# Optimization experiments

Measured on AMD Instinct MI355X. Metric: run time of the kernel, lower is better.

The kernel has to match this reference:

```python
import jax, jax.numpy as jnp
import numpy as np

N, E, F, H, C = 50000, 800000, 128, 4, 32
SLOPE_ATT = 0.2   # PyG GATConv default negative_slope for attention logits
SLOPE_ACT = 0.01  # torch leaky_relu default between layers


def setup_inputs() -> dict:
    key = jax.random.key(0)
    ks = jax.random.split(key, 12)
    sc = 0.1
    return {
        "x": jax.random.normal(ks[0], (N, F), jnp.float32),
        "edge_index": jax.random.randint(ks[1], (2, E), 0, N, dtype=jnp.int32),
        "W1": jax.random.normal(ks[2], (F, H * C), jnp.float32) * sc,
        "a_src1": jax.random.normal(ks[3], (H, C), jnp.float32) * sc,
        "a_dst1": jax.random.normal(ks[4], (H, C), jnp.float32) * sc,
        "b1": jnp.zeros((H * C,), jnp.float32),
        "W2": jax.random.normal(ks[5], (H * C, H * C), jnp.float32) * sc,
        "a_src2": jax.random.normal(ks[6], (H, C), jnp.float32) * sc,
        "a_dst2": jax.random.normal(ks[7], (H, C), jnp.float32) * sc,
        "b2": jnp.zeros((H * C,), jnp.float32),
        "Wfc": jax.random.normal(ks[8], (H * C, 1), jnp.float32) * sc,
        "bfc": jnp.zeros((1,), jnp.float32),
    }


def gat_layer(x, src, dst, W, a_src, a_dst, bias):
    """PyG-style GATConv: per-head linear, edge attention with leaky_relu,
    segment-softmax over incoming edges of each dst node, scatter-add aggregate."""
    n = x.shape[0]
    h = (x @ W).reshape(n, H, C)                       # [N,H,C]
    att_s = jnp.einsum('nhc,hc->nh', h, a_src)         # per-node src logits
    att_d = jnp.einsum('nhc,hc->nh', h, a_dst)         # per-node dst logits
    e = jax.nn.leaky_relu(att_s[src] + att_d[dst], SLOPE_ATT)   # [Etot,H]
    m = jax.ops.segment_max(e, dst, num_segments=n)    # stable softmax per dst
    e = jnp.exp(e - m[dst])
    z = jax.ops.segment_sum(e, dst, num_segments=n)
    alpha = e / (z[dst] + 1e-16)                       # [Etot,H]
    out = jax.ops.segment_sum(alpha[:, :, None] * h[src], dst, num_segments=n)
    return out.reshape(n, H * C) + bias                # concat heads + bias


def reference(x, edge_index, W1, a_src1, a_dst1, b1, W2, a_src2, a_dst2, b2, Wfc, bfc):
    loops = jnp.arange(N, dtype=edge_index.dtype)      # PyG adds self-loops
    src = jnp.concatenate([edge_index[0], loops])
    dst = jnp.concatenate([edge_index[1], loops])
    h = jax.nn.leaky_relu(gat_layer(x, src, dst, W1, a_src1, a_dst1, b1), SLOPE_ACT)
    h = jax.nn.leaky_relu(gat_layer(h, src, dst, W2, a_src2, a_dst2, b2), SLOPE_ACT)
    return (h @ Wfc + bfc).squeeze(-1)                 # [N]
```

## Files before the change

kernel.cpp:

```cpp
#include <hip/hip_runtime.h>
#include <hip/hip_fp16.h>

#define FD 128

typedef __attribute__((ext_vector_type(8))) short bf16x8;
typedef __attribute__((ext_vector_type(4))) float f32x4;

__device__ __forceinline__ float lrelu(float x, float s){ return x > 0.f ? x : s*x; }

__device__ __forceinline__ unsigned short f2bf(float f){
  unsigned u = __builtin_bit_cast(unsigned, f);
  return (unsigned short)((u + 0x7FFFu + ((u >> 16) & 1u)) >> 16);
}
__device__ __forceinline__ float bf2f(unsigned short h){
  unsigned u = ((unsigned)h) << 16;
  return __builtin_bit_cast(float, u);
}


__global__ __launch_bounds__(256) void count_wprep_kernel(const int* __restrict__ dst,
    int* __restrict__ counts, int E, unsigned rscale, int nchunk, int nbc,
    const float* __restrict__ W1, const float* __restrict__ W2,
    const float* __restrict__ aS1, const float* __restrict__ aD1,
    const float* __restrict__ aS2, const float* __restrict__ aD2,
    unsigned short* __restrict__ WT1, unsigned short* __restrict__ WT2)
{
  int b = blockIdx.x;
  if (b < nbc){
    int xcd = b & 7, chunk = b >> 3;
    int nv = E >> 2;
    for (int v = chunk*256 + threadIdx.x; v < nv; v += nchunk*256){
      int4 d4 = ((const int4*)dst)[v];
      #pragma unroll
      for (int t = 0; t < 4; ++t){
        int d = (&d4.x)[t];
        unsigned r = (unsigned)(((unsigned long long)(unsigned)d * rscale) >> 32);
        if ((int)r == xcd) atomicAdd(&counts[d], 1);
      }
    }
    if (chunk == 0 && threadIdx.x < (E & 3)){
      int i = (E & ~3) + threadIdx.x;
      int d = dst[i];
      unsigned r = (unsigned)(((unsigned long long)(unsigned)d * rscale) >> 32);
      if ((int)r == xcd) atomicAdd(&counts[d], 1);
    }
    return;
  }
  int id = (b - nbc)*256 + threadIdx.x;
  if (id < 32768){
    const float* W = (id < 16384) ? W1 : W2;
    unsigned short* T = (id < 16384) ? WT1 : WT2;
    int idx = id & 16383;
    int k = idx >> 7, c = idx & 127;
    int w = ((c & 7) << 4) | (c >> 3);
    int si = w*128 + (k ^ ((w & 7) << 3));
    float v = W[idx];
    unsigned short h = f2bf(v);
    T[si] = h;
    T[18432 + si] = f2bf(v - bf2f(h));
  } else if (id < 34816){
    int id2 = id - 32768;
    int layer = id2 >> 10;
    int id3 = id2 & 1023;
    int k = id3 >> 3, cc = id3 & 7;
    const float* W  = layer ? W2 : W1;
    const float* av = (cc < 4) ? (layer ? aS2 : aS1) : (layer ? aD2 : aD1);
    unsigned short* T = layer ? WT2 : WT1;
    int h = cc & 3, base = h*32;
    float acc = 0.f;
    #pragma unroll 8
    for (int c = 0; c < 32; ++c) acc += W[k*FD + base + c] * av[base + c];
    int w = 128 + cc;
    int si = w*128 + (k ^ ((w & 7) << 3));
    unsigned short hh = f2bf(acc);
    T[si] = hh;
    T[18432 + si] = f2bf(acc - bf2f(hh));
  } else if (id < 36864){
    int id2 = id - 34816;
    int layer = id2 >> 10;
    int id3 = id2 & 1023;
    int w = 136 + (id3 >> 7), k = id3 & 127;
    unsigned short* T = layer ? WT2 : WT1;
    int si = w*128 + (k ^ ((w & 7) << 3));
    T[si] = 0;
    T[18432 + si] = 0;
  }
}

__global__ __launch_bounds__(512) void scan1_kernel(const int* __restrict__ counts,
    int* __restrict__ offsets, int* __restrict__ blocksum, int n){
  __shared__ int wsum[8];
  int tid = threadIdx.x, lane = tid & 63, wv = tid >> 6;
  int i = blockIdx.x*512 + tid;
  int v = (i < n) ? counts[i] + 1 : 0;
  int incl = v;
  #pragma unroll
  for (int off = 1; off < 64; off <<= 1){
    int t = __shfl_up(incl, off);
    if (lane >= off) incl += t;
  }
  if (lane == 63) wsum[wv] = incl;
  __syncthreads();
  if (wv == 0 && lane < 8){
    int s = wsum[lane];
    #pragma unroll
    for (int off = 1; off < 8; off <<= 1){
      int t = __shfl_up(s, off);
      if (lane >= off) s += t;
    }
    wsum[lane] = s;
  }
  __syncthreads();
  int woff = (wv > 0) ? wsum[wv-1] : 0;
  incl += woff;
  if (i < n) offsets[i] = incl;
  if (tid == 511) blocksum[blockIdx.x] = incl;
}

__global__ __launch_bounds__(64) void scan2_kernel(int* __restrict__ blocksum,
    int* __restrict__ offsets, int nb, int n){
  int lane = threadIdx.x;
  int i0 = 2*lane, i1 = 2*lane + 1;
  int v0 = (i0 < nb) ? blocksum[i0] : 0;
  int v1 = (i1 < nb) ? blocksum[i1] : 0;
  int pair = v0 + v1;
  int incl = pair;
  #pragma unroll
  for (int off = 1; off < 64; off <<= 1){
    int t = __shfl_up(incl, off);
    if (lane >= off) incl += t;
  }
  int excl = incl - pair;
  if (i0 < nb) blocksum[i0] = excl;
  if (i1 < nb) blocksum[i1] = excl + v0;
  if (lane == 63) offsets[n] = incl;
}

__global__ __launch_bounds__(512) void scan3_kernel(const int* __restrict__ counts,
    int* __restrict__ offsets, const int* __restrict__ blocksum,
    int* __restrict__ csr, int n){
  int i = blockIdx.x*512 + threadIdx.x;
  if (i >= n) return;
  int v = counts[i] + 1;
  int gl = offsets[i] + blocksum[blockIdx.x];
  offsets[i] = gl - v;
  csr[gl - 1] = i;
}

__global__ __launch_bounds__(256) void fill_part_kernel(const int* __restrict__ ei,
    const int* __restrict__ offsets, int* __restrict__ counts, int* __restrict__ csr,
    int E, unsigned rscale, int nchunk){
  int b = blockIdx.x;
  int xcd = b & 7, chunk = b >> 3;
  int nv = E >> 2;
  for (int v = chunk*256 + threadIdx.x; v < nv; v += nchunk*256){
    int4 s4 = ((const int4*)ei)[v];
    int4 d4 = ((const int4*)(ei + E))[v];
    #pragma unroll
    for (int t = 0; t < 4; ++t){
      int d = (&d4.x)[t];
      unsigned r = (unsigned)(((unsigned long long)(unsigned)d * rscale) >> 32);
      if ((int)r == xcd){
        int c = atomicSub(&counts[d], 1) - 1;
        csr[offsets[d] + c] = (&s4.x)[t];
      }
    }
  }
  if (chunk == 0 && threadIdx.x < (E & 3)){
    int i = (E & ~3) + threadIdx.x;
    int d = ei[E + i];
    unsigned r = (unsigned)(((unsigned long long)(unsigned)d * rscale) >> 32);
    if ((int)r == xcd){
      int c = atomicSub(&counts[d], 1) - 1;
      csr[offsets[d] + c] = ei[i];
    }
  }
}

template<int SPLITIN>
__global__ __launch_bounds__(256) void gemm_mfma_kernel(
    const float* __restrict__ Xf,
    const unsigned short* __restrict__ Xh, const unsigned short* __restrict__ Xl,
    const unsigned short* __restrict__ WT,
    uint4* __restrict__ H16, float* __restrict__ attS, float* __restrict__ attD, int n)
{
  __shared__ unsigned short smem[36864];
  int tid = threadIdx.x;
  int wv = tid >> 6, lane = tid & 63;
  int g = lane >> 4, r = lane & 15;
  int rbase = blockIdx.x*64 + wv*16;
  int arow = rbase + r; if (arow >= n) arow = n - 1;

  {
    const uint4* src = (const uint4*)WT;
    uint4* dst = (uint4*)smem;
    #pragma unroll
    for (int i = 0; i < 18; ++i) dst[tid + i*256] = src[tid + i*256];
  }

  bf16x8 Ah[4], Al[4];
  if (SPLITIN){
    const bf16x8* ph = (const bf16x8*)(Xh + (size_t)arow*FD);
    const bf16x8* pl = (const bf16x8*)(Xl + (size_t)arow*FD);
    #pragma unroll
    for (int kc = 0; kc < 4; ++kc){ Ah[kc] = ph[kc*4 + g]; Al[kc] = pl[kc*4 + g]; }
  } else {
    const float4* px = (const float4*)(Xf + (size_t)arow*FD);
    #pragma unroll
    for (int kc = 0; kc < 4; ++kc){
      float4 x0 = px[(kc*4 + g)*2];
      float4 x1 = px[(kc*4 + g)*2 + 1];
      float xs[8] = {x0.x,x0.y,x0.z,x0.w,x1.x,x1.y,x1.z,x1.w};
      #pragma unroll
      for (int t = 0; t < 8; ++t){
        unsigned short hh = f2bf(xs[t]);
        Ah[kc][t] = (short)hh;
        Al[kc][t] = (short)f2bf(xs[t] - bf2f(hh));
      }
    }
  }

  __syncthreads();

  f32x4 acc[9];
  #pragma unroll
  for (int ct = 0; ct < 9; ++ct) acc[ct] = (f32x4){0.f,0.f,0.f,0.f};

  #pragma unroll
  for (int ct = 0; ct < 9; ++ct){
    int wrow = ct*16 + r;
    int sw = (wrow & 7) << 3;
    #pragma unroll
    for (int kc = 0; kc < 4; ++kc){
      int kidx = (kc*32 + g*8) ^ sw;
      bf16x8 Bh = *(const bf16x8*)&smem[wrow*128 + kidx];
      bf16x8 Bl = *(const bf16x8*)&smem[18432 + wrow*128 + kidx];
      acc[ct] = __builtin_amdgcn_mfma_f32_16x16x32_bf16(Ah[kc], Bh, acc[ct], 0, 0, 0);
      acc[ct] = __builtin_amdgcn_mfma_f32_16x16x32_bf16(Ah[kc], Bl, acc[ct], 0, 0, 0);
      acc[ct] = __builtin_amdgcn_mfma_f32_16x16x32_bf16(Al[kc], Bh, acc[ct], 0, 0, 0);
    }
  }

  #pragma unroll
  for (int j = 0; j < 4; ++j){
    int row = rbase + g*4 + j;
    if (row < n){
      __half2 p0 = __float22half2_rn(make_float2(acc[0][j], acc[1][j]));
      __half2 p1 = __float22half2_rn(make_float2(acc[2][j], acc[3][j]));
      __half2 p2 = __float22half2_rn(make_float2(acc[4][j], acc[5][j]));
      __half2 p3 = __float22half2_rn(make_float2(acc[6][j], acc[7][j]));
      uint4 pk;
      pk.x = __builtin_bit_cast(unsigned, p0);
      pk.y = __builtin_bit_cast(unsigned, p1);
      pk.z = __builtin_bit_cast(unsigned, p2);
      pk.w = __builtin_bit_cast(unsigned, p3);
      H16[(size_t)row*16 + r] = pk;
      if (r < 4)      attS[row*4 + r]       = acc[8][j];
      else if (r < 8) attD[row*4 + (r - 4)] = acc[8][j];
    }
  }
}

template<int OUT>
__global__ __launch_bounds__(256) void agg_kernel(
    const uint2* __restrict__ H16, const float* __restrict__ attS, const float* __restrict__ attD,
    const int* __restrict__ csr, const int* __restrict__ offsets,
    const float* __restrict__ bias, const float* __restrict__ wfc, const float* __restrict__ bfc,
    unsigned short* __restrict__ oh, unsigned short* __restrict__ ol,
    float* __restrict__ out, int n)
{
  __shared__ float lds[4][64*5];
  int wid = (int)((blockIdx.x * (size_t)blockDim.x + threadIdx.x) >> 6);
  int lane = threadIdx.x & 63;
  if (wid >= n) return;
  int g = lane >> 4, r = lane & 15;
  int selA = (r >> 3) & 1;
  float* wl = lds[threadIdx.x >> 6];
  int* wli = (int*)wl;

  int start = offsets[wid], end = offsets[wid+1];
  float4 ad4 = ((const float4*)attD)[wid];

  float z0=0.f, z1=0.f, z2=0.f, z3=0.f;
  float acc[8];
  #pragma unroll
  for (int k = 0; k < 8; ++k) acc[k] = 0.f;

  for (int base2 = start; base2 < end; base2 += 64){
    int cnt = end - base2; if (cnt > 64) cnt = 64;
    float p0,p1,p2,p3; int sb = 0;
    if (lane < cnt){
      int s = csr[base2 + lane];
      sb = s << 5;
      float4 as4 = ((const float4*)attS)[s];
      p0 = __expf(lrelu(as4.x + ad4.x, 0.2f));
      p1 = __expf(lrelu(as4.y + ad4.y, 0.2f));
      p2 = __expf(lrelu(as4.z + ad4.z, 0.2f));
      p3 = __expf(lrelu(as4.w + ad4.w, 0.2f));
    } else { p0=p1=p2=p3=0.f; }
    z0+=p0; z1+=p1; z2+=p2; z3+=p3;
    wli[lane*5]  = sb;
    wl[lane*5+1] = p0; wl[lane*5+2] = p1; wl[lane*5+3] = p2; wl[lane*5+4] = p3;
    asm volatile("s_waitcnt lgkmcnt(0)" ::: "memory");
    __builtin_amdgcn_sched_barrier(0);
    for (int jj = g; jj < cnt; jj += 4){
      int sbj  = wli[jj*5];
      float pA = wl[jj*5 + 1 + selA];
      float pB = wl[jj*5 + 3 + selA];
      uint2 u0 = H16[(unsigned)(sbj + r)];
      uint2 u1 = H16[(unsigned)(sbj + 16 + r)];
      float2 a0 = __half22float2(__builtin_bit_cast(__half2, u0.x));
      float2 a1 = __half22float2(__builtin_bit_cast(__half2, u0.y));
      float2 a2 = __half22float2(__builtin_bit_cast(__half2, u1.x));
      float2 a3 = __half22float2(__builtin_bit_cast(__half2, u1.y));
      acc[0] += pA*a0.x; acc[1] += pA*a0.y; acc[2] += pA*a1.x; acc[3] += pA*a1.y;
      acc[4] += pB*a2.x; acc[5] += pB*a2.y; acc[6] += pB*a3.x; acc[7] += pB*a3.y;
    }
    __builtin_amdgcn_sched_barrier(0);
  }

  #pragma unroll
  for (int off = 32; off >= 1; off >>= 1){
    z0+=__shfl_xor(z0,off); z1+=__shfl_xor(z1,off);
    z2+=__shfl_xor(z2,off); z3+=__shfl_xor(z3,off);
  }
  #pragma unroll
  for (int k = 0; k < 8; ++k){
    acc[k] += __shfl_xor(acc[k], 16);
    acc[k] += __shfl_xor(acc[k], 32);
  }
  float o0 = g==0?acc[0]:g==1?acc[2]:g==2?acc[4]:acc[6];
  float o1 = g==0?acc[1]:g==1?acc[3]:g==2?acc[5]:acc[7];
  int ch0 = ((g>>1)<<6) + (r<<2) + ((g&1)<<1);
  float zz = (g < 2) ? ((r<8)? z0 : z1) : ((r<8)? z2 : z3);
  float inv = 1.f / (zz + 1e-16f);
  float2 b2v = ((const float2*)bias)[ch0 >> 1];
  o0 = lrelu(o0*inv + b2v.x, 0.01f);
  o1 = lrelu(o1*inv + b2v.y, 0.01f);
  if (OUT){
    float2 w2v = ((const float2*)wfc)[ch0 >> 1];
    float t = o0*w2v.x + o1*w2v.y;
    #pragma unroll
    for (int off = 32; off >= 1; off >>= 1) t += __shfl_xor(t, off);
    if (lane == 0) out[wid] = t + bfc[0];
  } else {
    unsigned short h0 = f2bf(o0);
    unsigned short h1 = f2bf(o1);
    unsigned short l0 = f2bf(o0 - bf2f(h0));
    unsigned short l1 = f2bf(o1 - bf2f(h1));
    ((unsigned*)oh)[(size_t)wid*64 + (ch0>>1)] = (unsigned)h0 | ((unsigned)h1 << 16);
    ((unsigned*)ol)[(size_t)wid*64 + (ch0>>1)] = (unsigned)l0 | ((unsigned)l1 << 16);
  }
}

extern "C" void kernel_launch(void* const* d_in, const int* in_sizes, int n_in,
                              void* d_out, int out_size, void* d_ws, size_t ws_size,
                              hipStream_t stream)
{
  const float* x   = (const float*)d_in[0];
  const int*   ei  = (const int*)d_in[1];
  const float* W1  = (const float*)d_in[2];
  const float* aS1 = (const float*)d_in[3];
  const float* aD1 = (const float*)d_in[4];
  const float* b1  = (const float*)d_in[5];
  const float* W2  = (const float*)d_in[6];
  const float* aS2 = (const float*)d_in[7];
  const float* aD2 = (const float*)d_in[8];
  const float* b2  = (const float*)d_in[9];
  const float* Wfc = (const float*)d_in[10];
  const float* bfc = (const float*)d_in[11];
  float* out = (float*)d_out;

  int n = in_sizes[0] / FD;
  int E = in_sizes[1] / 2;
  int etot = E + n;
  unsigned rscale = (unsigned)(((8ULL << 32) + n - 1) / (unsigned long long)n);

  char* p = (char*)d_ws;
  auto alloc = [&](size_t bytes)->void*{
    void* r = (void*)p;
    p += (bytes + 255) & ~(size_t)255;
    return r;
  };
  int* counts    = (int*)alloc((size_t)n * 4);
  int* offsets   = (int*)alloc((size_t)(n + 1) * 4);
  int* blocksum  = (int*)alloc(1024 * 4);
  int* csr       = (int*)alloc((size_t)etot * 4);
  float* attS1   = (float*)alloc((size_t)n * 4 * 4);
  float* attD1   = (float*)alloc((size_t)n * 4 * 4);
  float* attS2   = (float*)alloc((size_t)n * 4 * 4);
  float* attD2   = (float*)alloc((size_t)n * 4 * 4);
  unsigned short* WT1 = (unsigned short*)alloc(36864*2);
  unsigned short* WT2 = (unsigned short*)alloc(36864*2);
  uint4* H16     = (uint4*)alloc((size_t)n * FD * 2);
  unsigned short* H2h = (unsigned short*)alloc((size_t)n * FD * 2);
  unsigned short* H2l = (unsigned short*)alloc((size_t)n * FD * 2);

  hipMemsetAsync(counts, 0, (size_t)n * 4, stream);

  const int NB_PART = 512;
  int nsb = (n + 511) / 512;
  count_wprep_kernel<<<NB_PART + 144, 256, 0, stream>>>(ei + E, counts, E, rscale,
      NB_PART/8, NB_PART, W1, W2, aS1, aD1, aS2, aD2, WT1, WT2);
  scan1_kernel<<<nsb, 512, 0, stream>>>(counts, offsets, blocksum, n);
  scan2_kernel<<<1, 64, 0, stream>>>(blocksum, offsets, nsb, n);
  scan3_kernel<<<nsb, 512, 0, stream>>>(counts, offsets, blocksum, csr, n);
  fill_part_kernel<<<NB_PART, 256, 0, stream>>>(ei, offsets, counts, csr, E, rscale, NB_PART/8);

  int gb = (n + 63) / 64;
  int ab = (int)(((size_t)n * 64 + 255) / 256);

  gemm_mfma_kernel<0><<<gb, 256, 0, stream>>>(x, nullptr, nullptr, WT1,
                                              H16, attS1, attD1, n);
  agg_kernel<0><<<ab, 256, 0, stream>>>((const uint2*)H16, attS1, attD1, csr, offsets,
                                        b1, nullptr, nullptr, H2h, H2l, nullptr, n);
  gemm_mfma_kernel<1><<<gb, 256, 0, stream>>>(nullptr, H2h, H2l, WT2,
                                              H16, attS2, attD2, n);
  agg_kernel<1><<<ab, 256, 0, stream>>>((const uint2*)H16, attS2, attD2, csr, offsets,
                                        b2, Wfc, bfc, nullptr, nullptr, out, n);
}
```

Measured before the change: 204.2 us.

## Split aggregation into per-head passes with one wave per node-head

The aggregation kernel now runs four passes, one per attention head. Each wave handles a single node and head and gathers only that head's 64-byte slice of each source row with 16-byte loads, 16 edges per iteration. The intent is to shrink each pass's gather working set so it fits better in cache, and to cut per-edge exp work to one head. In exchange, the CSR indices and offsets are read four times, the final FC output is staged per head and summed in an extra small kernel, and only 4 lanes do the epilogue.

```diff
diff --git a/kernel.cpp b/kernel.cpp
--- a/kernel.cpp
+++ b/kernel.cpp
@@ -262,94 +262,110 @@
 }
 
 template<int OUT>
-__global__ __launch_bounds__(256) void agg_kernel(
-    const uint2* __restrict__ H16, const float* __restrict__ attS, const float* __restrict__ attD,
+__global__ __launch_bounds__(256) void agg_pass_kernel(
+    const uint4* __restrict__ H16, const float* __restrict__ attS, const float* __restrict__ attD,
     const int* __restrict__ csr, const int* __restrict__ offsets,
-    const float* __restrict__ bias, const float* __restrict__ wfc, const float* __restrict__ bfc,
-    unsigned short* __restrict__ oh, unsigned short* __restrict__ ol,
-    float* __restrict__ out, int n)
+    const float* __restrict__ bias, const float* __restrict__ wfc,
+    uint4* __restrict__ oh, uint4* __restrict__ ol,
+    float* __restrict__ outstage, int n, int bpp)
 {
-  __shared__ float lds[4][64*5];
-  int wid = (int)((blockIdx.x * (size_t)blockDim.x + threadIdx.x) >> 6);
+  __shared__ float lds[4][128];
+  int pass = blockIdx.x / bpp;
+  int bin  = blockIdx.x - pass*bpp;
+  int wid  = bin*4 + (threadIdx.x >> 6);
   int lane = threadIdx.x & 63;
   if (wid >= n) return;
-  int g = lane >> 4, r = lane & 15;
-  int selA = (r >> 3) & 1;
+  int q = lane & 3, grp = lane >> 2;
   float* wl = lds[threadIdx.x >> 6];
   int* wli = (int*)wl;
 
   int start = offsets[wid], end = offsets[wid+1];
-  float4 ad4 = ((const float4*)attD)[wid];
-
-  float z0=0.f, z1=0.f, z2=0.f, z3=0.f;
+  float adQ = attD[wid*4 + pass];
+
+  float z = 0.f;
   float acc[8];
   #pragma unroll
   for (int k = 0; k < 8; ++k) acc[k] = 0.f;
 
   for (int base2 = start; base2 < end; base2 += 64){
     int cnt = end - base2; if (cnt > 64) cnt = 64;
-    float p0,p1,p2,p3; int sb = 0;
+    float p = 0.f; int sb = 0;
     if (lane < cnt){
       int s = csr[base2 + lane];
-      sb = s << 5;
-      float4 as4 = ((const float4*)attS)[s];
-      p0 = __expf(lrelu(as4.x + ad4.x, 0.2f));
-      p1 = __expf(lrelu(as4.y + ad4.y, 0.2f));
-      p2 = __expf(lrelu(as4.z + ad4.z, 0.2f));
-      p3 = __expf(lrelu(as4.w + ad4.w, 0.2f));
-    } else { p0=p1=p2=p3=0.f; }
-    z0+=p0; z1+=p1; z2+=p2; z3+=p3;
-    wli[lane*5]  = sb;
-    wl[lane*5+1] = p0; wl[lane*5+2] = p1; wl[lane*5+3] = p2; wl[lane*5+4] = p3;
+      sb = (s << 4) + (pass << 2);
+      p = __expf(lrelu(attS[s*4 + pass] + adQ, 0.2f));
+    }
+    z += p;
+    wli[lane*2]  = sb;
+    wl[lane*2+1] = p;
     asm volatile("s_waitcnt lgkmcnt(0)" ::: "memory");
     __builtin_amdgcn_sched_barrier(0);
-    for (int jj = g; jj < cnt; jj += 4){
-      int sbj  = wli[jj*5];
-      float pA = wl[jj*5 + 1 + selA];
-      float pB = wl[jj*5 + 3 + selA];
-      uint2 u0 = H16[(unsigned)(sbj + r)];
-      uint2 u1 = H16[(unsigned)(sbj + 16 + r)];
-      float2 a0 = __half22float2(__builtin_bit_cast(__half2, u0.x));
-      float2 a1 = __half22float2(__builtin_bit_cast(__half2, u0.y));
-      float2 a2 = __half22float2(__builtin_bit_cast(__half2, u1.x));
-      float2 a3 = __half22float2(__builtin_bit_cast(__half2, u1.y));
-      acc[0] += pA*a0.x; acc[1] += pA*a0.y; acc[2] += pA*a1.x; acc[3] += pA*a1.y;
-      acc[4] += pB*a2.x; acc[5] += pB*a2.y; acc[6] += pB*a3.x; acc[7] += pB*a3.y;
+    for (int jj = grp; jj < cnt; jj += 16){
+      int sbj  = wli[jj*2];
+      float pj = wl[jj*2+1];
+      uint4 u = H16[(unsigned)(sbj + q)];
+      float2 t0 = __half22float2(__builtin_bit_cast(__half2, u.x));
+      float2 t1 = __half22float2(__builtin_bit_cast(__half2, u.y));
+      float2 t2 = __half22float2(__builtin_bit_cast(__half2, u.z));
+      float2 t3 = __half22float2(__builtin_bit_cast(__half2, u.w));
+      acc[0] += pj*t0.x; acc[1] += pj*t0.y;
+      acc[2] += pj*t1.x; acc[3] += pj*t1.y;
+      acc[4] += pj*t2.x; acc[5] += pj*t2.y;
+      acc[6] += pj*t3.x; acc[7] += pj*t3.y;
     }
     __builtin_amdgcn_sched_barrier(0);
   }
 
   #pragma unroll
-  for (int off = 32; off >= 1; off >>= 1){
-    z0+=__shfl_xor(z0,off); z1+=__shfl_xor(z1,off);
-    z2+=__shfl_xor(z2,off); z3+=__shfl_xor(z3,off);
-  }
+  for (int off = 32; off >= 1; off >>= 1) z += __shfl_xor(z, off);
   #pragma unroll
   for (int k = 0; k < 8; ++k){
+    acc[k] += __shfl_xor(acc[k], 4);
+    acc[k] += __shfl_xor(acc[k], 8);
     acc[k] += __shfl_xor(acc[k], 16);
     acc[k] += __shfl_xor(acc[k], 32);
   }
-  float o0 = g==0?acc[0]:g==1?acc[2]:g==2?acc[4]:acc[6];
-  float o1 = g==0?acc[1]:g==1?acc[3]:g==2?acc[5]:acc[7];
-  int ch0 = ((g>>1)<<6) + (r<<2) + ((g&1)<<1);
-  float zz = (g < 2) ? ((r<8)? z0 : z1) : ((r<8)? z2 : z3);
-  float inv = 1.f / (zz + 1e-16f);
-  float2 b2v = ((const float2*)bias)[ch0 >> 1];
-  o0 = lrelu(o0*inv + b2v.x, 0.01f);
-  o1 = lrelu(o1*inv + b2v.y, 0.01f);
-  if (OUT){
-    float2 w2v = ((const float2*)wfc)[ch0 >> 1];
-    float t = o0*w2v.x + o1*w2v.y;
-    #pragma unroll
-    for (int off = 32; off >= 1; off >>= 1) t += __shfl_xor(t, off);
-    if (lane == 0) out[wid] = t + bfc[0];
-  } else {
-    unsigned short h0 = f2bf(o0);
-    unsigned short h1 = f2bf(o1);
-    unsigned short l0 = f2bf(o0 - bf2f(h0));
-    unsigned short l1 = f2bf(o1 - bf2f(h1));
-    ((unsigned*)oh)[(size_t)wid*64 + (ch0>>1)] = (unsigned)h0 | ((unsigned)h1 << 16);
-    ((unsigned*)ol)[(size_t)wid*64 + (ch0>>1)] = (unsigned)l0 | ((unsigned)l1 << 16);
+
+  if (lane < 4){
+    float inv = 1.f / (z + 1e-16f);
+    int ch0 = (pass << 5) + (lane << 3);
+    const float4* b4 = (const float4*)bias;
+    float4 b0 = b4[ch0 >> 2], b1 = b4[(ch0 >> 2) + 1];
+    float o[8];
+    o[0]=lrelu(acc[0]*inv+b0.x,0.01f); o[1]=lrelu(acc[1]*inv+b0.y,0.01f);
+    o[2]=lrelu(acc[2]*inv+b0.z,0.01f); o[3]=lrelu(acc[3]*inv+b0.w,0.01f);
+    o[4]=lrelu(acc[4]*inv+b1.x,0.01f); o[5]=lrelu(acc[5]*inv+b1.y,0.01f);
+    o[6]=lrelu(acc[6]*inv+b1.z,0.01f); o[7]=lrelu(acc[7]*inv+b1.w,0.01f);
+    if (OUT){
+      const float4* w4 = (const float4*)wfc;
+      float4 w0 = w4[ch0 >> 2], w1 = w4[(ch0 >> 2) + 1];
+      float t = o[0]*w0.x + o[1]*w0.y + o[2]*w0.z + o[3]*w0.w
+              + o[4]*w1.x + o[5]*w1.y + o[6]*w1.z + o[7]*w1.w;
+      t += __shfl_xor(t, 1);
+      t += __shfl_xor(t, 2);
+      if (lane == 0) outstage[wid*4 + pass] = t;
+    } else {
+      unsigned hh[8], ll[8];
+      #pragma unroll
+      for (int i = 0; i < 8; ++i){
+        unsigned short h = f2bf(o[i]);
+        hh[i] = h; ll[i] = f2bf(o[i] - bf2f(h));
+      }
+      uint4 ph = {hh[0]|(hh[1]<<16), hh[2]|(hh[3]<<16), hh[4]|(hh[5]<<16), hh[6]|(hh[7]<<16)};
+      uint4 pl = {ll[0]|(ll[1]<<16), ll[2]|(ll[3]<<16), ll[4]|(ll[5]<<16), ll[6]|(ll[7]<<16)};
+      int oi = wid*16 + (pass << 2) + lane;
+      oh[oi] = ph;
+      ol[oi] = pl;
+    }
+  }
+}
+
+__global__ __launch_bounds__(256) void fcsum_kernel(const float4* __restrict__ outstage,
+    const float* __restrict__ bfc, float* __restrict__ out, int n){
+  int i = blockIdx.x*256 + threadIdx.x;
+  if (i < n){
+    float4 v = outstage[i];
+    out[i] = v.x + v.y + v.z + v.w + bfc[0];
   }
 }
 
@@ -390,6 +406,7 @@
   float* attD1   = (float*)alloc((size_t)n * 4 * 4);
   float* attS2   = (float*)alloc((size_t)n * 4 * 4);
   float* attD2   = (float*)alloc((size_t)n * 4 * 4);
+  float* outstage= (float*)alloc((size_t)n * 4 * 4);
   unsigned short* WT1 = (unsigned short*)alloc(36864*2);
   unsigned short* WT2 = (unsigned short*)alloc(36864*2);
   uint4* H16     = (uint4*)alloc((size_t)n * FD * 2);
@@ -408,14 +425,15 @@
   fill_part_kernel<<<NB_PART, 256, 0, stream>>>(ei, offsets, counts, csr, E, rscale, NB_PART/8);
 
   int gb = (n + 63) / 64;
-  int ab = (int)(((size_t)n * 64 + 255) / 256);
+  int bpp = (n + 3) / 4;
 
   gemm_mfma_kernel<0><<<gb, 256, 0, stream>>>(x, nullptr, nullptr, WT1,
                                               H16, attS1, attD1, n);
-  agg_kernel<0><<<ab, 256, 0, stream>>>((const uint2*)H16, attS1, attD1, csr, offsets,
-                                        b1, nullptr, nullptr, H2h, H2l, nullptr, n);
+  agg_pass_kernel<0><<<4*bpp, 256, 0, stream>>>(H16, attS1, attD1, csr, offsets,
+                                b1, nullptr, (uint4*)H2h, (uint4*)H2l, nullptr, n, bpp);
   gemm_mfma_kernel<1><<<gb, 256, 0, stream>>>(nullptr, H2h, H2l, WT2,
                                               H16, attS2, attD2, n);
-  agg_kernel<1><<<ab, 256, 0, stream>>>((const uint2*)H16, attS2, attD2, csr, offsets,
-                                        b2, Wfc, bfc, nullptr, nullptr, out, n);
-}
+  agg_pass_kernel<1><<<4*bpp, 256, 0, stream>>>(H16, attS2, attD2, csr, offsets,
+                                b2, Wfc, nullptr, nullptr, outstage, n, bpp);
+  fcsum_kernel<<<(n + 255)/256, 256, 0, stream>>>((const float4*)outstage, bfc, out, n);
+}
```

Result: slower. 319.6 us (+56.6%).

## Store layer-1 output as single fp16 buffer and fold scan2 into scan3

Applied to the files above, without the earlier changes.

The intermediate activation between the two GAT layers is now written as one fp16 array instead of a bf16 hi/lo split pair, halving its write and read traffic. The second GEMM converts the fp16 values back to float and splits them into bf16 hi/lo in registers. Separately, the single-block scan2 launch is removed: each scan3 block sums the preceding block totals itself and the last thread writes offsets[n]. The change trades activation precision (fp16 instead of roughly fp32-equivalent split bf16) and adds redundant prefix work per block in exchange for one fewer launch and less memory traffic.

```diff
diff --git a/kernel.cpp b/kernel.cpp
--- a/kernel.cpp
+++ b/kernel.cpp
@@ -117,34 +117,27 @@
   if (tid == 511) blocksum[blockIdx.x] = incl;
 }
 
-__global__ __launch_bounds__(64) void scan2_kernel(int* __restrict__ blocksum,
-    int* __restrict__ offsets, int nb, int n){
-  int lane = threadIdx.x;
-  int i0 = 2*lane, i1 = 2*lane + 1;
-  int v0 = (i0 < nb) ? blocksum[i0] : 0;
-  int v1 = (i1 < nb) ? blocksum[i1] : 0;
-  int pair = v0 + v1;
-  int incl = pair;
-  #pragma unroll
-  for (int off = 1; off < 64; off <<= 1){
-    int t = __shfl_up(incl, off);
-    if (lane >= off) incl += t;
-  }
-  int excl = incl - pair;
-  if (i0 < nb) blocksum[i0] = excl;
-  if (i1 < nb) blocksum[i1] = excl + v0;
-  if (lane == 63) offsets[n] = incl;
-}
-
 __global__ __launch_bounds__(512) void scan3_kernel(const int* __restrict__ counts,
     int* __restrict__ offsets, const int* __restrict__ blocksum,
-    int* __restrict__ csr, int n){
-  int i = blockIdx.x*512 + threadIdx.x;
+    int* __restrict__ csr, int n, int nsb){
+  __shared__ int boff_s;
+  int tid = threadIdx.x, b = blockIdx.x;
+  if (tid < 64){
+    int s = 0;
+    for (int j = tid; j < b; j += 64) s += blocksum[j];
+    #pragma unroll
+    for (int off = 32; off >= 1; off >>= 1) s += __shfl_xor(s, off);
+    if (tid == 0) boff_s = s;
+  }
+  __syncthreads();
+  int i = b*512 + tid;
   if (i >= n) return;
+  int boff = boff_s;
   int v = counts[i] + 1;
-  int gl = offsets[i] + blocksum[blockIdx.x];
+  int gl = offsets[i] + boff;
   offsets[i] = gl - v;
   csr[gl - 1] = i;
+  if (i == n - 1) offsets[n] = gl;
 }
 
 __global__ __launch_bounds__(256) void fill_part_kernel(const int* __restrict__ ei,
@@ -179,8 +172,7 @@
 
 template<int SPLITIN>
 __global__ __launch_bounds__(256) void gemm_mfma_kernel(
-    const float* __restrict__ Xf,
-    const unsigned short* __restrict__ Xh, const unsigned short* __restrict__ Xl,
+    const float* __restrict__ Xf, const unsigned short* __restrict__ X16,
     const unsigned short* __restrict__ WT,
     uint4* __restrict__ H16, float* __restrict__ attS, float* __restrict__ attD, int n)
 {
@@ -200,10 +192,22 @@
 
   bf16x8 Ah[4], Al[4];
   if (SPLITIN){
-    const bf16x8* ph = (const bf16x8*)(Xh + (size_t)arow*FD);
-    const bf16x8* pl = (const bf16x8*)(Xl + (size_t)arow*FD);
-    #pragma unroll
-    for (int kc = 0; kc < 4; ++kc){ Ah[kc] = ph[kc*4 + g]; Al[kc] = pl[kc*4 + g]; }
+    const uint4* ph = (const uint4*)(X16 + (size_t)arow*FD);
+    #pragma unroll
+    for (int kc = 0; kc < 4; ++kc){
+      uint4 u = ph[kc*4 + g];
+      float2 f0 = __half22float2(__builtin_bit_cast(__half2, u.x));
+      float2 f1 = __half22float2(__builtin_bit_cast(__half2, u.y));
+      float2 f2 = __half22float2(__builtin_bit_cast(__half2, u.z));
+      float2 f3 = __half22float2(__builtin_bit_cast(__half2, u.w));
+      float xs[8] = {f0.x,f0.y,f1.x,f1.y,f2.x,f2.y,f3.x,f3.y};
+      #pragma unroll
+      for (int t = 0; t < 8; ++t){
+        unsigned short hh = f2bf(xs[t]);
+        Ah[kc][t] = (short)hh;
+        Al[kc][t] = (short)f2bf(xs[t] - bf2f(hh));
+      }
+    }
   } else {
     const float4* px = (const float4*)(Xf + (size_t)arow*FD);
     #pragma unroll
@@ -266,8 +270,7 @@
     const uint2* __restrict__ H16, const float* __restrict__ attS, const float* __restrict__ attD,
     const int* __restrict__ csr, const int* __restrict__ offsets,
     const float* __restrict__ bias, const float* __restrict__ wfc, const float* __restrict__ bfc,
-    unsigned short* __restrict__ oh, unsigned short* __restrict__ ol,
-    float* __restrict__ out, int n)
+    unsigned* __restrict__ o16, float* __restrict__ out, int n)
 {
   __shared__ float lds[4][64*5];
   int wid = (int)((blockIdx.x * (size_t)blockDim.x + threadIdx.x) >> 6);
@@ -344,12 +347,8 @@
     for (int off = 32; off >= 1; off >>= 1) t += __shfl_xor(t, off);
     if (lane == 0) out[wid] = t + bfc[0];
   } else {
-    unsigned short h0 = f2bf(o0);
-    unsigned short h1 = f2bf(o1);
-    unsigned short l0 = f2bf(o0 - bf2f(h0));
-    unsigned short l1 = f2bf(o1 - bf2f(h1));
-    ((unsigned*)oh)[(size_t)wid*64 + (ch0>>1)] = (unsigned)h0 | ((unsigned)h1 << 16);
-    ((unsigned*)ol)[(size_t)wid*64 + (ch0>>1)] = (unsigned)l0 | ((unsigned)l1 << 16);
+    __half2 hv = __float22half2_rn(make_float2(o0, o1));
+    o16[(size_t)wid*64 + (ch0 >> 1)] = __builtin_bit_cast(unsigned, hv);
   }
 }
 
@@ -393,8 +392,7 @@
   unsigned short* WT1 = (unsigned short*)alloc(36864*2);
   unsigned short* WT2 = (unsigned short*)alloc(36864*2);
   uint4* H16     = (uint4*)alloc((size_t)n * FD * 2);
-  unsigned short* H2h = (unsigned short*)alloc((size_t)n * FD * 2);
-  unsigned short* H2l = (unsigned short*)alloc((size_t)n * FD * 2);
+  unsigned short* H2 = (unsigned short*)alloc((size_t)n * FD * 2);
 
   hipMemsetAsync(counts, 0, (size_t)n * 4, stream);
 
@@ -403,19 +401,18 @@
   count_wprep_kernel<<<NB_PART + 144, 256, 0, stream>>>(ei + E, counts, E, rscale,
       NB_PART/8, NB_PART, W1, W2, aS1, aD1, aS2, aD2, WT1, WT2);
   scan1_kernel<<<nsb, 512, 0, stream>>>(counts, offsets, blocksum, n);
-  scan2_kernel<<<1, 64, 0, stream>>>(blocksum, offsets, nsb, n);
-  scan3_kernel<<<nsb, 512, 0, stream>>>(counts, offsets, blocksum, csr, n);
+  scan3_kernel<<<nsb, 512, 0, stream>>>(counts, offsets, blocksum, csr, n, nsb);
   fill_part_kernel<<<NB_PART, 256, 0, stream>>>(ei, offsets, counts, csr, E, rscale, NB_PART/8);
 
   int gb = (n + 63) / 64;
   int ab = (int)(((size_t)n * 64 + 255) / 256);
 
-  gemm_mfma_kernel<0><<<gb, 256, 0, stream>>>(x, nullptr, nullptr, WT1,
+  gemm_mfma_kernel<0><<<gb, 256, 0, stream>>>(x, nullptr, WT1,
                                               H16, attS1, attD1, n);
   agg_kernel<0><<<ab, 256, 0, stream>>>((const uint2*)H16, attS1, attD1, csr, offsets,
-                                        b1, nullptr, nullptr, H2h, H2l, nullptr, n);
-  gemm_mfma_kernel<1><<<gb, 256, 0, stream>>>(nullptr, H2h, H2l, WT2,
+                                        b1, nullptr, nullptr, (unsigned*)H2, nullptr, n);
+  gemm_mfma_kernel<1><<<gb, 256, 0, stream>>>(nullptr, H2, WT2,
                                               H16, attS2, attD2, n);
   agg_kernel<1><<<ab, 256, 0, stream>>>((const uint2*)H16, attS2, attD2, csr, offsets,
-                                        b2, Wfc, bfc, nullptr, nullptr, out, n);
-}
+                                        b2, Wfc, bfc, nullptr, out, n);
+}
```

After: 201.3 us. No clear change (-1.4%).
